# Kernel optimization log

Measured on AMD Instinct MI355X. Metric: run time of the kernel, lower is better.

## Reference

```python
import jax, jax.numpy as jnp
import numpy as np

WEIGHT_BIT = 8
BIAS_BIT = 32
STRIDE = (1, 1)
PAD = ((1, 1), (1, 1))


def setup_inputs() -> dict:
    key = jax.random.key(0)
    k1, k2, k3, k4 = jax.random.split(key, 4)
    N, Cin, Cout, K, H, W = 64, 256, 256, 3, 28, 28
    x_q = jax.random.randint(k1, (N, Cin, H, W), 0, 255, dtype=jnp.int32)
    scale_x = jax.random.uniform(k2, (1,), dtype=jnp.float32) * 0.1 + 0.01
    weight = jax.random.normal(k3, (Cout, Cin, K, K), dtype=jnp.float32) * 0.05
    bias = jax.random.normal(k4, (Cout,), dtype=jnp.float32) * 0.1
    return {"x_q": x_q, "scale_x": scale_x, "weight": weight, "bias": bias}


def _quant_weight_per_channel(w, bit):
    # symmetric per-output-channel quantization from min/max (ZeroQ SymmetricQuantFunction)
    n = 2 ** (bit - 1) - 1  # 127 for 8-bit
    wf = w.reshape(w.shape[0], -1)
    sat = jnp.maximum(jnp.abs(wf.min(axis=1)), jnp.abs(wf.max(axis=1)))
    scale = jnp.clip(sat, 1e-8, None) / n  # [Cout]
    w_q = jnp.clip(jnp.round(w / scale[:, None, None, None]), -n - 1, n).astype(jnp.int32)
    return w_q, scale


def reference(x_q, scale_x, weight, bias):
    # fake-quantize weight per output channel
    w_q, scale_w = _quant_weight_per_channel(weight, WEIGHT_BIT)  # int32 [Cout,Cin,K,K], f32 [Cout]
    scale_out = scale_w * scale_x[0]  # [Cout]
    # quantize bias with the combined scale (bias_bit=32)
    nb = float(2 ** (BIAS_BIT - 1) - 1)
    b_q = jnp.clip(jnp.round(bias / scale_out), -nb - 1.0, nb).astype(jnp.int32)  # [Cout]
    out_q = jax.lax.conv_general_dilated(
        x_q, w_q, window_strides=STRIDE, padding=PAD,
        dimension_numbers=("NCHW", "OIHW", "NCHW"),
    ) + b_q[None, :, None, None]
    return out_q, scale_out.reshape(1, -1, 1, 1)
```

## Files before the change

kernel.cpp:

```cpp
#include <hip/hip_runtime.h>
#include <hip/hip_bf16.h>

typedef int   i32x4 __attribute__((ext_vector_type(4)));
typedef int   int4v __attribute__((ext_vector_type(4)));

#define N_IMG 64
#define CIN   256
#define COUT  256
#define HH    28
#define WW    28
#define PH    30
#define PW    30
#define M_TOT (N_IMG*HH*WW)
#define OUT_ELEMS (N_IMG*COUT*HH*WW)

#define XT_BYTES   ((size_t)N_IMG*PH*PW*CIN)
#define WT_OFF     (XT_BYTES)
#define WT_BYTES   ((size_t)9*COUT*CIN)
#define BQ_OFF     (WT_OFF + WT_BYTES)

#define GLD16(g, l) __builtin_amdgcn_global_load_lds( \
    (const __attribute__((address_space(1))) void*)(g), \
    (__attribute__((address_space(3))) void*)(l), 16, 0, 0)

__global__ __launch_bounds__(256) void prep(const int* __restrict__ xq,
                                            const float* __restrict__ weight,
                                            const float* __restrict__ scale_x,
                                            const float* __restrict__ bias,
                                            signed char* __restrict__ xt,
                                            signed char* __restrict__ wt,
                                            int* __restrict__ bq,
                                            float* __restrict__ out_tail) {
    __shared__ int xs[28*260];
    const int b = blockIdx.x;
    const int t = threadIdx.x;

    if (b < N_IMG*PH) {
        const int n = b / PH, py = b % PH;
        signed char* dst = xt + ((size_t)(n*PH + py))*PW*CIN;
        if (py == 0 || py == PH-1) {
            int* d4 = (int*)dst;
            for (int i = t; i < PW*CIN/4; i += 256) d4[i] = 0x81818181;
            return;
        }
        const int h = py - 1;
        const int* src = xq + (size_t)n*CIN*HH*WW + h*WW;
        for (int i = t; i < CIN*7; i += 256) {
            const int ci = i / 7, q = i % 7;
            const int4v v = *(const int4v*)(src + ci*HH*WW + q*4);
            xs[(4*q    )*260 + ci] = v.x;
            xs[(4*q + 1)*260 + ci] = v.y;
            xs[(4*q + 2)*260 + ci] = v.z;
            xs[(4*q + 3)*260 + ci] = v.w;
        }
        __syncthreads();
        for (int i = t; i < PW*CIN/4; i += 256) {
            const int px = i >> 6, ci0 = (i & 63) << 2;
            unsigned int o;
            if (px == 0 || px == PW-1) o = 0x81818181u;
            else {
                const int4v v = *(const int4v*)&xs[(px - 1)*260 + ci0];
                const unsigned int b0 = (unsigned char)(v.x - 127);
                const unsigned int b1 = (unsigned char)(v.y - 127);
                const unsigned int b2 = (unsigned char)(v.z - 127);
                const unsigned int b3 = (unsigned char)(v.w - 127);
                o = b0 | (b1 << 8) | (b2 << 16) | (b3 << 24);
            }
            ((unsigned int*)dst)[i] = o;
        }
        return;
    }

    float* red  = (float*)xs;
    int*   sred = (int*)xs + 256;
    const int co = b - N_IMG*PH;
    const float* wrow = weight + (size_t)co*CIN*9;
    float wv[9];
    float mx = 0.f;
    for (int it = 0; it < 9; ++it) {
        float v = wrow[it*256 + t];
        wv[it] = v;
        mx = fmaxf(mx, fabsf(v));
    }
    red[t] = mx;
    __syncthreads();
    for (int s = 128; s > 0; s >>= 1) {
        if (t < s) red[t] = fmaxf(red[t], red[t+s]);
        __syncthreads();
    }
    const float scale = fmaxf(red[0], 1e-8f) / 127.f;
    int isum = 0;
    for (int it = 0; it < 9; ++it) {
        const int i = it*256 + t;
        const int ci = i / 9, rs = i % 9;
        float q = rintf(wv[it] / scale);
        q = fminf(fmaxf(q, -128.f), 127.f);
        const int qi = (int)q;
        isum += qi;
        wt[(size_t)rs*COUT*CIN + co*CIN + ci] = (signed char)qi;
    }
    sred[t] = isum;
    __syncthreads();
    for (int s = 128; s > 0; s >>= 1) {
        if (t < s) sred[t] += sred[t+s];
        __syncthreads();
    }
    if (t == 0) {
        const float so = scale * scale_x[0];
        out_tail[co] = so;
        bq[co] = (int)rintf(bias[co] / so) + 127 * sred[0];
    }
}

__global__ __launch_bounds__(256, 2) void conv_mfma(const signed char* __restrict__ xt,
                                                    const signed char* __restrict__ wt,
                                                    const int* __restrict__ bq,
                                                    float* __restrict__ out) {
    __shared__ signed char Ash[2*16384];
    __shared__ signed char Bsh[2*16384];
    const int d = threadIdx.x;
    const int w4 = d >> 6;
    const int lane = d & 63, lr = lane & 15, kg = lane >> 4;
    const int wm = w4 >> 1, wn = w4 & 1;
    const int bx = blockIdx.x;
    const int mb = (bx & 7)*49 + (bx >> 3);
    const int m0 = mb << 7;
    const int co0 = blockIdx.y << 7;

    const int srow = d >> 3;
    const int skc  = (d & 7) ^ (srow & 7);
    const signed char* aS = wt + (size_t)(co0 + srow)*CIN + (skc << 4);
    const signed char* bS[4];
#pragma unroll
    for (int j = 0; j < 4; ++j) {
        const int m = m0 + srow + j*32;
        const int n = m / 784, hw = m % 784, h = hw / 28, wq = hw % 28;
        bS[j] = xt + ((size_t)((n*PH + h)*PW + wq))*CIN + (skc << 4);
    }
    const int w4off = w4 << 10;

    i32x4 acc[4][4] = {};

    const int a0 = (wm*64 + lr)*128 + ((kg ^ (lr & 7)) << 4);
    const int b0 = (wn*64 + lr)*128 + ((kg ^ (lr & 7)) << 4);

#define STAGE(T_, P_) do { \
    const int tap_ = (T_) >> 1, c_ = (T_) & 1; \
    const int r3_ = (tap_*171) >> 9; \
    const int ao_ = tap_*(COUT*CIN) + (c_ << 7); \
    const int bo_ = ((r3_*PW + (tap_ - r3_*3)) << 8) + (c_ << 7); \
    GLD16(aS + ao_,         Ash + (P_)*16384 +         w4off); \
    GLD16(aS + ao_ +  8192, Ash + (P_)*16384 +  4096 + w4off); \
    GLD16(aS + ao_ + 16384, Ash + (P_)*16384 +  8192 + w4off); \
    GLD16(aS + ao_ + 24576, Ash + (P_)*16384 + 12288 + w4off); \
    GLD16(bS[0] + bo_,      Bsh + (P_)*16384 +         w4off); \
    GLD16(bS[1] + bo_,      Bsh + (P_)*16384 +  4096 + w4off); \
    GLD16(bS[2] + bo_,      Bsh + (P_)*16384 +  8192 + w4off); \
    GLD16(bS[3] + bo_,      Bsh + (P_)*16384 + 12288 + w4off); \
} while (0)

#define COMPUTE(P_) do { \
    const signed char* A_ = Ash + (P_)*16384; \
    const signed char* B_ = Bsh + (P_)*16384; \
    _Pragma("unroll") \
    for (int ks = 0; ks < 2; ++ks) { \
        const int ar = a0 ^ (ks << 6); \
        const int br = b0 ^ (ks << 6); \
        i32x4 af[4], bf[4]; \
        _Pragma("unroll") \
        for (int mr = 0; mr < 4; ++mr) \
            af[mr] = *(const i32x4*)&A_[ar + mr*2048]; \
        _Pragma("unroll") \
        for (int nr = 0; nr < 4; ++nr) \
            bf[nr] = *(const i32x4*)&B_[br + nr*2048]; \
        _Pragma("unroll") \
        for (int mr = 0; mr < 4; ++mr) \
            _Pragma("unroll") \
            for (int nr = 0; nr < 4; ++nr) \
                acc[mr][nr] = __builtin_amdgcn_mfma_i32_16x16x64_i8( \
                    af[mr], bf[nr], acc[mr][nr], 0, 0, 0); \
    } \
} while (0)

#define SYNCPT() do { \
    asm volatile("s_waitcnt vmcnt(0) lgkmcnt(0)" ::: "memory"); \
    __builtin_amdgcn_s_barrier(); \
    __builtin_amdgcn_sched_barrier(0); \
} while (0)

    STAGE(0, 0);
#pragma unroll 1
    for (int tt = 0; tt < 18; tt += 2) {
        SYNCPT();
        STAGE(tt + 1, 1);
        COMPUTE(0);
        SYNCPT();
        if (tt < 16) STAGE(tt + 2, 0);
        COMPUTE(1);
    }

#pragma unroll
    for (int nr = 0; nr < 4; ++nr) {
        const int mm = m0 + wn*64 + nr*16 + lr;
        const int nn = mm / 784, hw2 = mm % 784;
        float* orow = out + (size_t)nn*COUT*784 + hw2;
#pragma unroll
        for (int mr = 0; mr < 4; ++mr) {
            const int co = co0 + wm*64 + mr*16 + kg*4;
#pragma unroll
            for (int rg = 0; rg < 4; ++rg)
                orow[(size_t)(co + rg)*784] = (float)(acc[mr][nr][rg] + bq[co + rg]);
        }
    }
#undef STAGE
#undef COMPUTE
#undef SYNCPT
}

extern "C" void kernel_launch(void* const* d_in, const int* in_sizes, int n_in,
                              void* d_out, int out_size, void* d_ws, size_t ws_size,
                              hipStream_t stream) {
    const int*   xq      = (const int*)d_in[0];
    const float* scale_x = (const float*)d_in[1];
    const float* weight  = (const float*)d_in[2];
    const float* bias    = (const float*)d_in[3];
    float* out = (float*)d_out;

    signed char* xt = (signed char*)d_ws;
    signed char* wt = (signed char*)((char*)d_ws + WT_OFF);
    int*         bq = (int*)((char*)d_ws + BQ_OFF);

    hipLaunchKernelGGL(prep, dim3(N_IMG*PH + COUT), dim3(256), 0, stream,
                       xq, weight, scale_x, bias, xt, wt, bq, out + OUT_ELEMS);
    hipLaunchKernelGGL(conv_mfma, dim3(M_TOT/128, COUT/128), dim3(256), 0, stream,
                       xt, wt, bq, out);
}
```

Measured before the change: 66.90 us.

## Switch conv GEMM to triple-buffered K=64 stages with partial vmcnt waits

Halves the K chunk per stage to 64 bytes and uses three LDS buffers instead of two. This keeps two stages of global-to-LDS loads in flight while computing. Barriers now wait only until the older stage's loads land (vmcnt(4)) rather than draining everything, so memory latency overlaps with MFMA work. The cost is twice as many barriers per tile and less compute per sync; total LDS use drops to 48KB.

Result: slower. 78.70 us (+17.6%).

```diff
diff --git a/kernel.cpp b/kernel.cpp
--- a/kernel.cpp
+++ b/kernel.cpp
@@ -116,88 +116,81 @@
                                                     const signed char* __restrict__ wt,
                                                     const int* __restrict__ bq,
                                                     float* __restrict__ out) {
-    __shared__ signed char Ash[2*16384];
-    __shared__ signed char Bsh[2*16384];
+    __shared__ signed char Ash[3*8192];
+    __shared__ signed char Bsh[3*8192];
     const int d = threadIdx.x;
+    const int lane = d & 63, lr = lane & 15, kg = lane >> 4;
     const int w4 = d >> 6;
-    const int lane = d & 63, lr = lane & 15, kg = lane >> 4;
     const int wm = w4 >> 1, wn = w4 & 1;
     const int bx = blockIdx.x;
     const int mb = (bx & 7)*49 + (bx >> 3);
     const int m0 = mb << 7;
     const int co0 = blockIdx.y << 7;
 
-    const int srow = d >> 3;
-    const int skc  = (d & 7) ^ (srow & 7);
+    const int srow = d >> 2;
+    const int skc  = (d & 3) ^ (srow & 3);
     const signed char* aS = wt + (size_t)(co0 + srow)*CIN + (skc << 4);
-    const signed char* bS[4];
-#pragma unroll
-    for (int j = 0; j < 4; ++j) {
-        const int m = m0 + srow + j*32;
-        const int n = m / 784, hw = m % 784, h = hw / 28, wq = hw % 28;
-        bS[j] = xt + ((size_t)((n*PH + h)*PW + wq))*CIN + (skc << 4);
-    }
-    const int w4off = w4 << 10;
+    const signed char* bS0;
+    const signed char* bS1;
+    {
+        int m = m0 + srow;
+        int n = m / 784, hw = m % 784, h = hw / 28, wq = hw % 28;
+        bS0 = xt + ((size_t)((n*PH + h)*PW + wq))*CIN + (skc << 4);
+        m += 64;
+        n = m / 784; hw = m % 784; h = hw / 28; wq = hw % 28;
+        bS1 = xt + ((size_t)((n*PH + h)*PW + wq))*CIN + (skc << 4);
+    }
+    const int d16 = d << 4;
 
     i32x4 acc[4][4] = {};
 
-    const int a0 = (wm*64 + lr)*128 + ((kg ^ (lr & 7)) << 4);
-    const int b0 = (wn*64 + lr)*128 + ((kg ^ (lr & 7)) << 4);
+    const int arb = (wm*64 + lr)*64 + ((kg ^ (lr & 3)) << 4);
+    const int brb = (wn*64 + lr)*64 + ((kg ^ (lr & 3)) << 4);
 
 #define STAGE(T_, P_) do { \
-    const int tap_ = (T_) >> 1, c_ = (T_) & 1; \
+    const int tap_ = (T_) >> 2, c_ = (T_) & 3; \
     const int r3_ = (tap_*171) >> 9; \
-    const int ao_ = tap_*(COUT*CIN) + (c_ << 7); \
-    const int bo_ = ((r3_*PW + (tap_ - r3_*3)) << 8) + (c_ << 7); \
-    GLD16(aS + ao_,         Ash + (P_)*16384 +         w4off); \
-    GLD16(aS + ao_ +  8192, Ash + (P_)*16384 +  4096 + w4off); \
-    GLD16(aS + ao_ + 16384, Ash + (P_)*16384 +  8192 + w4off); \
-    GLD16(aS + ao_ + 24576, Ash + (P_)*16384 + 12288 + w4off); \
-    GLD16(bS[0] + bo_,      Bsh + (P_)*16384 +         w4off); \
-    GLD16(bS[1] + bo_,      Bsh + (P_)*16384 +  4096 + w4off); \
-    GLD16(bS[2] + bo_,      Bsh + (P_)*16384 +  8192 + w4off); \
-    GLD16(bS[3] + bo_,      Bsh + (P_)*16384 + 12288 + w4off); \
+    const int ao_ = tap_*(COUT*CIN) + (c_ << 6); \
+    const int bo_ = ((r3_*PW + (tap_ - r3_*3)) << 8) + (c_ << 6); \
+    GLD16(aS + ao_,             Ash + (P_)*8192 +        d16); \
+    GLD16(aS + ao_ + 64*CIN,    Ash + (P_)*8192 + 4096 + d16); \
+    GLD16(bS0 + bo_,            Bsh + (P_)*8192 +        d16); \
+    GLD16(bS1 + bo_,            Bsh + (P_)*8192 + 4096 + d16); \
 } while (0)
 
 #define COMPUTE(P_) do { \
-    const signed char* A_ = Ash + (P_)*16384; \
-    const signed char* B_ = Bsh + (P_)*16384; \
+    const signed char* A_ = Ash + (P_)*8192; \
+    const signed char* B_ = Bsh + (P_)*8192; \
+    i32x4 af[4], bf[4]; \
     _Pragma("unroll") \
-    for (int ks = 0; ks < 2; ++ks) { \
-        const int ar = a0 ^ (ks << 6); \
-        const int br = b0 ^ (ks << 6); \
-        i32x4 af[4], bf[4]; \
-        _Pragma("unroll") \
-        for (int mr = 0; mr < 4; ++mr) \
-            af[mr] = *(const i32x4*)&A_[ar + mr*2048]; \
+    for (int mr = 0; mr < 4; ++mr) af[mr] = *(const i32x4*)&A_[arb + mr*1024]; \
+    _Pragma("unroll") \
+    for (int nr = 0; nr < 4; ++nr) bf[nr] = *(const i32x4*)&B_[brb + nr*1024]; \
+    _Pragma("unroll") \
+    for (int mr = 0; mr < 4; ++mr) \
         _Pragma("unroll") \
         for (int nr = 0; nr < 4; ++nr) \
-            bf[nr] = *(const i32x4*)&B_[br + nr*2048]; \
-        _Pragma("unroll") \
-        for (int mr = 0; mr < 4; ++mr) \
-            _Pragma("unroll") \
-            for (int nr = 0; nr < 4; ++nr) \
-                acc[mr][nr] = __builtin_amdgcn_mfma_i32_16x16x64_i8( \
-                    af[mr], bf[nr], acc[mr][nr], 0, 0, 0); \
-    } \
+            acc[mr][nr] = __builtin_amdgcn_mfma_i32_16x16x64_i8( \
+                af[mr], bf[nr], acc[mr][nr], 0, 0, 0); \
 } while (0)
 
-#define SYNCPT() do { \
-    asm volatile("s_waitcnt vmcnt(0) lgkmcnt(0)" ::: "memory"); \
+#define GATE(N_) do { \
+    asm volatile("s_waitcnt vmcnt(" #N_ ")" ::: "memory"); \
     __builtin_amdgcn_s_barrier(); \
     __builtin_amdgcn_sched_barrier(0); \
 } while (0)
 
     STAGE(0, 0);
+    STAGE(1, 1);
 #pragma unroll 1
-    for (int tt = 0; tt < 18; tt += 2) {
-        SYNCPT();
-        STAGE(tt + 1, 1);
-        COMPUTE(0);
-        SYNCPT();
-        if (tt < 16) STAGE(tt + 2, 0);
-        COMPUTE(1);
-    }
+    for (int tt = 0; tt < 33; tt += 3) {
+        GATE(4); STAGE(tt + 2, 2); COMPUTE(0);
+        GATE(4); STAGE(tt + 3, 0); COMPUTE(1);
+        GATE(4); STAGE(tt + 4, 1); COMPUTE(2);
+    }
+    GATE(4); STAGE(35, 2); COMPUTE(0);
+    GATE(4); COMPUTE(1);
+    GATE(0); COMPUTE(2);
 
 #pragma unroll
     for (int nr = 0; nr < 4; ++nr) {
@@ -214,7 +207,7 @@
     }
 #undef STAGE
 #undef COMPUTE
-#undef SYNCPT
+#undef GATE
 }
 
 extern "C" void kernel_launch(void* const* d_in, const int* in_sizes, int n_in,
```
